# Optimization experiments

Hardware: AMD Instinct MI355X
Metric: run time of the kernel (lower is better)

Reference implementation:

```python
import jax, jax.numpy as jnp
import numpy as np

NB_SAMPLES = 16
GAMMA = 0.04       # also the noise_intensity passed to randomArgmax
ALPHA = 1.0
EPS = 1e-10


def setup_inputs() -> dict:
    key = jax.random.key(0)
    k1, k2, k3 = jax.random.split(key, 3)
    B, H, W, K = 8, 128, 128, 32
    zbuf = jax.random.normal(k1, (B, H, W, K), dtype=jnp.float32)
    prob_map = jax.random.uniform(k2, (B, H, W, K), dtype=jnp.float32)
    mask = jnp.ones((B, H, W, K), dtype=jnp.float32)
    zfar = jnp.ones((1,), dtype=jnp.float32)
    znear = jnp.zeros((1,), dtype=jnp.float32)
    # gaussian noise normally drawn inside randomArgmax.forward; made explicit for determinism
    noise = jax.random.normal(k3, (NB_SAMPLES, B, H, W, K + 1), dtype=jnp.float32)
    return {"zbuf": zbuf, "zfar": zfar, "znear": znear,
            "prob_map": prob_map, "mask": mask, "noise": noise}


def _random_argmax(z, noise, sigma):
    # z: [B,H,W,C]; noise: [S,B,H,W,C]
    C = z.shape[-1]
    z_pert = z[None] + sigma * noise                       # [S,B,H,W,C]
    idx = jnp.argmax(z_pert, axis=-1)                      # first-max, matches torch.max
    weights = jax.nn.one_hot(idx, C, dtype=z.dtype)        # [S,B,H,W,C]
    return weights.mean(axis=0)                            # [B,H,W,C]


def reference(zbuf, zfar, znear, prob_map, mask, noise):
    # inverse depth, masked
    z_inv = (zfar - zbuf) / (zfar - znear) * mask          # [B,H,W,K]
    z_inv_max = jnp.maximum(jnp.max(z_inv, axis=-1, keepdims=True), EPS)
    z_map = GAMMA / ALPHA * jnp.log(1e-12 + prob_map) + z_inv - z_inv_max
    bg = EPS - z_inv_max                                   # background channel [B,H,W,1]
    z_map = jnp.concatenate([z_map, bg], axis=-1)          # [B,H,W,K+1]
    return _random_argmax(z_map, noise, GAMMA)
```

## Files before the change

kernel.cpp:

```cpp
#include <hip/hip_runtime.h>
#include <cstdint>


#define NPIX    131072
#define KCH     32
#define CCH     33
#define SAMP    16
#define TPB     128
#define TILE_F  (TPB * CCH)
#define TILE_V4 (TILE_F / 4)
#define FULL_J  (TILE_V4 / TPB)
#define REM     (TILE_V4 % TPB)

__global__ __launch_bounds__(TPB)
void gauss_agg_kernel(const float* __restrict__ zbuf,
                      const float* __restrict__ zfar_p,
                      const float* __restrict__ znear_p,
                      const float* __restrict__ prob,
                      const float* __restrict__ mask,
                      const float* __restrict__ noise,
                      float* __restrict__ out)
{
#pragma clang fp contract(off)
    __shared__ float buf[TILE_F];
    const int tid = threadIdx.x;
    const int p0  = blockIdx.x * TPB;
    const size_t p = (size_t)p0 + tid;

    const float zfar  = zfar_p[0];
    const float znear = znear_p[0];
    const float denom = zfar - znear;

    float zb[KCH], pm[KCH], mk[KCH];
    {
        const float4* zb4 = reinterpret_cast<const float4*>(zbuf + p * KCH);
        const float4* pm4 = reinterpret_cast<const float4*>(prob + p * KCH);
        const float4* mk4 = reinterpret_cast<const float4*>(mask + p * KCH);
        #pragma unroll
        for (int i = 0; i < KCH / 4; ++i) {
            float4 a = zb4[i], b = pm4[i], c = mk4[i];
            zb[4*i+0] = a.x; zb[4*i+1] = a.y; zb[4*i+2] = a.z; zb[4*i+3] = a.w;
            pm[4*i+0] = b.x; pm[4*i+1] = b.y; pm[4*i+2] = b.z; pm[4*i+3] = b.w;
            mk[4*i+0] = c.x; mk[4*i+1] = c.y; mk[4*i+2] = c.z; mk[4*i+3] = c.w;
        }
    }

    float4 r[FULL_J + 1];
    {
        const float4* g4 = reinterpret_cast<const float4*>(
            noise + (size_t)p0 * CCH);
        #pragma unroll
        for (int j = 0; j < FULL_J; ++j) r[j] = g4[tid + j * TPB];
        if (tid < REM) r[FULL_J] = g4[tid + FULL_J * TPB];
    }

    float z_inv[KCH];
    float zmax = 1e-10f;
    #pragma unroll
    for (int k = 0; k < KCH; ++k) {
        float zi = ((zfar - zb[k]) / denom) * mk[k];
        z_inv[k] = zi;
        zmax = fmaxf(zmax, zi);
    }

    float z_map[CCH];
    #pragma unroll
    for (int k = 0; k < KCH; ++k) {
        float lg = logf(1e-12f + pm[k]);
        z_map[k] = ((0.04f * lg) + z_inv[k]) - zmax;
    }
    z_map[KCH] = 1e-10f - zmax;

    int acc[CCH];
    #pragma unroll
    for (int c = 0; c < CCH; ++c) acc[c] = 0;

    for (int s = 0; s < SAMP; ++s) {
        if (s) __syncthreads();
        {
            float4* l4 = reinterpret_cast<float4*>(buf);
            #pragma unroll
            for (int j = 0; j < FULL_J; ++j) l4[tid + j * TPB] = r[j];
            if (tid < REM) l4[tid + FULL_J * TPB] = r[FULL_J];
        }
        __syncthreads();
        if (s + 1 < SAMP) {
            const float4* g4 = reinterpret_cast<const float4*>(
                noise + ((size_t)(s + 1) * NPIX + p0) * CCH);
            #pragma unroll
            for (int j = 0; j < FULL_J; ++j) r[j] = g4[tid + j * TPB];
            if (tid < REM) r[FULL_J] = g4[tid + FULL_J * TPB];
        }
        const float* nb = buf + tid * CCH;
        float best = z_map[0] + (0.04f * nb[0]);
        int bi = 0;
        #pragma unroll
        for (int c = 1; c < CCH; ++c) {
            float v = z_map[c] + (0.04f * nb[c]);
            if (v > best) { best = v; bi = c; }
        }
        #pragma unroll
        for (int c = 0; c < CCH; ++c) acc[c] += (bi == c);
    }

    {
        const int rb = tid * CCH;
        #pragma unroll
        for (int c = 0; c < CCH; ++c) buf[rb + c] = (float)acc[c] * 0.0625f;
    }
    __syncthreads();
    {
        const float4* l4 = reinterpret_cast<const float4*>(buf);
        float4* o4 = reinterpret_cast<float4*>(out + (size_t)p0 * CCH);
        #pragma unroll
        for (int j = 0; j < FULL_J; ++j) o4[tid + j * TPB] = l4[tid + j * TPB];
        if (tid < REM) o4[tid + FULL_J * TPB] = l4[tid + FULL_J * TPB];
    }
}

extern "C" void kernel_launch(void* const* d_in, const int* in_sizes, int n_in,
                              void* d_out, int out_size, void* d_ws, size_t ws_size,
                              hipStream_t stream)
{
    const float* zbuf  = (const float*)d_in[0];
    const float* zfar  = (const float*)d_in[1];
    const float* znear = (const float*)d_in[2];
    const float* prob  = (const float*)d_in[3];
    const float* mask  = (const float*)d_in[4];
    const float* noise = (const float*)d_in[5];
    float* out = (float*)d_out;

    dim3 grid(NPIX / TPB), block(TPB);
    gauss_agg_kernel<<<grid, block, 0, stream>>>(zbuf, zfar, znear, prob, mask,
                                                 noise, out);
}
```

Measured before the change: 442.6 us.

## Double-buffer noise tile in LDS and prefetch next sample earlier

Splits the shared-memory noise tile into two buffers that alternate per sample, which removes the barrier at the top of each iteration. The global load of the next sample's noise is now issued before the current tile is written to shared memory, so it has more time to overlap with the argmax work. Noise loads become nontemporal and the sample loop is fully unrolled. The cost is twice the LDS per block and a second register set for prefetched noise, which can lower occupancy.

After: 455.0 us. +2.8%, slower.

```diff
diff --git a/kernel.cpp b/kernel.cpp
--- a/kernel.cpp
+++ b/kernel.cpp
@@ -12,6 +12,8 @@
 #define FULL_J  (TILE_V4 / TPB)
 #define REM     (TILE_V4 % TPB)
 
+typedef float f4 __attribute__((ext_vector_type(4)));
+
 __global__ __launch_bounds__(TPB)
 void gauss_agg_kernel(const float* __restrict__ zbuf,
                       const float* __restrict__ zfar_p,
@@ -22,7 +24,7 @@
                       float* __restrict__ out)
 {
 #pragma clang fp contract(off)
-    __shared__ float buf[TILE_F];
+    __shared__ float buf[2][TILE_F];
     const int tid = threadIdx.x;
     const int p0  = blockIdx.x * TPB;
     const size_t p = (size_t)p0 + tid;
@@ -33,25 +35,27 @@
 
     float zb[KCH], pm[KCH], mk[KCH];
     {
-        const float4* zb4 = reinterpret_cast<const float4*>(zbuf + p * KCH);
-        const float4* pm4 = reinterpret_cast<const float4*>(prob + p * KCH);
-        const float4* mk4 = reinterpret_cast<const float4*>(mask + p * KCH);
+        const f4* zb4 = reinterpret_cast<const f4*>(zbuf + p * KCH);
+        const f4* pm4 = reinterpret_cast<const f4*>(prob + p * KCH);
+        const f4* mk4 = reinterpret_cast<const f4*>(mask + p * KCH);
         #pragma unroll
         for (int i = 0; i < KCH / 4; ++i) {
-            float4 a = zb4[i], b = pm4[i], c = mk4[i];
-            zb[4*i+0] = a.x; zb[4*i+1] = a.y; zb[4*i+2] = a.z; zb[4*i+3] = a.w;
-            pm[4*i+0] = b.x; pm[4*i+1] = b.y; pm[4*i+2] = b.z; pm[4*i+3] = b.w;
-            mk[4*i+0] = c.x; mk[4*i+1] = c.y; mk[4*i+2] = c.z; mk[4*i+3] = c.w;
+            f4 a = zb4[i], b = pm4[i], c = mk4[i];
+            #pragma unroll
+            for (int q = 0; q < 4; ++q) {
+                zb[4*i+q] = a[q]; pm[4*i+q] = b[q]; mk[4*i+q] = c[q];
+            }
         }
     }
 
-    float4 r[FULL_J + 1];
+    f4 r[2][FULL_J + 1];
     {
-        const float4* g4 = reinterpret_cast<const float4*>(
-            noise + (size_t)p0 * CCH);
+        const f4* g4 = reinterpret_cast<const f4*>(noise + (size_t)p0 * CCH);
         #pragma unroll
-        for (int j = 0; j < FULL_J; ++j) r[j] = g4[tid + j * TPB];
-        if (tid < REM) r[FULL_J] = g4[tid + FULL_J * TPB];
+        for (int j = 0; j < FULL_J; ++j)
+            r[0][j] = __builtin_nontemporal_load(&g4[tid + j * TPB]);
+        if (tid < REM)
+            r[0][FULL_J] = __builtin_nontemporal_load(&g4[tid + FULL_J * TPB]);
     }
 
     float z_inv[KCH];
@@ -62,7 +66,6 @@
         z_inv[k] = zi;
         zmax = fmaxf(zmax, zi);
     }
-
     float z_map[CCH];
     #pragma unroll
     for (int k = 0; k < KCH; ++k) {
@@ -75,23 +78,28 @@
     #pragma unroll
     for (int c = 0; c < CCH; ++c) acc[c] = 0;
 
+    #pragma unroll
     for (int s = 0; s < SAMP; ++s) {
-        if (s) __syncthreads();
+        const int cur = s & 1;
+        if (s + 1 < SAMP) {
+            const f4* g4 = reinterpret_cast<const f4*>(
+                noise + ((size_t)(s + 1) * NPIX + p0) * CCH);
+            #pragma unroll
+            for (int j = 0; j < FULL_J; ++j)
+                r[cur ^ 1][j] = __builtin_nontemporal_load(&g4[tid + j * TPB]);
+            if (tid < REM)
+                r[cur ^ 1][FULL_J] =
+                    __builtin_nontemporal_load(&g4[tid + FULL_J * TPB]);
+        }
         {
-            float4* l4 = reinterpret_cast<float4*>(buf);
+            f4* l4 = reinterpret_cast<f4*>(buf[cur]);
             #pragma unroll
-            for (int j = 0; j < FULL_J; ++j) l4[tid + j * TPB] = r[j];
-            if (tid < REM) l4[tid + FULL_J * TPB] = r[FULL_J];
+            for (int j = 0; j < FULL_J; ++j) l4[tid + j * TPB] = r[cur][j];
+            if (tid < REM) l4[tid + FULL_J * TPB] = r[cur][FULL_J];
         }
         __syncthreads();
-        if (s + 1 < SAMP) {
-            const float4* g4 = reinterpret_cast<const float4*>(
-                noise + ((size_t)(s + 1) * NPIX + p0) * CCH);
-            #pragma unroll
-            for (int j = 0; j < FULL_J; ++j) r[j] = g4[tid + j * TPB];
-            if (tid < REM) r[FULL_J] = g4[tid + FULL_J * TPB];
-        }
-        const float* nb = buf + tid * CCH;
+
+        const float* nb = buf[cur] + tid * CCH;
         float best = z_map[0] + (0.04f * nb[0]);
         int bi = 0;
         #pragma unroll
@@ -106,12 +114,12 @@
     {
         const int rb = tid * CCH;
         #pragma unroll
-        for (int c = 0; c < CCH; ++c) buf[rb + c] = (float)acc[c] * 0.0625f;
+        for (int c = 0; c < CCH; ++c) buf[0][rb + c] = (float)acc[c] * 0.0625f;
     }
     __syncthreads();
     {
-        const float4* l4 = reinterpret_cast<const float4*>(buf);
-        float4* o4 = reinterpret_cast<float4*>(out + (size_t)p0 * CCH);
+        const f4* l4 = reinterpret_cast<const f4*>(buf[0]);
+        f4* o4 = reinterpret_cast<f4*>(out + (size_t)p0 * CCH);
         #pragma unroll
         for (int j = 0; j < FULL_J; ++j) o4[tid + j * TPB] = l4[tid + j * TPB];
         if (tid < REM) o4[tid + FULL_J * TPB] = l4[tid + FULL_J * TPB];
```
